# Optimization experiments

Hardware: AMD Instinct MI355X
Metric: run time of the kernel (lower is better)

The kernel has to match this reference:

```python
import jax, jax.numpy as jnp
import numpy as np

B, N, K = 4, 4096, 16
D_POINTS, D_MODEL = 64, 256


def _ln(x, g, b, eps=1e-5):
    mu = jnp.mean(x, axis=-1, keepdims=True)
    var = jnp.mean((x - mu) ** 2, axis=-1, keepdims=True)
    return (x - mu) * jax.lax.rsqrt(var + eps) * g + b


def _gather(points, idx):
    # points: [B,N,C], idx: [B,N,K] -> [B,N,K,C]
    b = jnp.arange(points.shape[0])[:, None, None]
    return points[b, idx]


def setup_inputs() -> dict:
    key = jax.random.key(0)
    ks = jax.random.split(key, 16)
    std_qkv = np.sqrt(2.0 / D_MODEL).astype(np.float32)
    return {
        "xyz": jax.random.normal(ks[0], (B, N, 3), jnp.float32),
        "features": jax.random.normal(ks[1], (B, N, D_POINTS), jnp.float32),
        "W_pre": jax.random.normal(ks[2], (D_MODEL, D_POINTS), jnp.float32) * 0.02,
        "b_pre": jnp.zeros((D_MODEL,), jnp.float32),
        "W_post": jax.random.normal(ks[3], (D_POINTS, D_MODEL), jnp.float32) * 0.02,
        "b_post": jnp.zeros((D_POINTS,), jnp.float32),
        "Wp1": jax.random.normal(ks[4], (D_MODEL, 3), jnp.float32) * 0.02,
        "Wp2": jax.random.normal(ks[5], (D_MODEL, D_MODEL), jnp.float32) * 0.02,
        "Wa1": jax.random.normal(ks[6], (D_MODEL, D_MODEL), jnp.float32) * 0.02,
        "Wa2": jax.random.normal(ks[7], (D_MODEL, D_MODEL), jnp.float32) * 0.02,
        "WQ": jax.random.normal(ks[8], (D_MODEL, D_MODEL), jnp.float32) * std_qkv,
        "WK": jax.random.normal(ks[9], (D_MODEL, D_MODEL), jnp.float32) * std_qkv,
        "WV": jax.random.normal(ks[10], (D_MODEL, D_MODEL), jnp.float32) * std_qkv,
        "Wproj": jax.random.normal(ks[11], (D_MODEL, D_MODEL), jnp.float32) * 0.02,
        "g_dm": jnp.ones((D_MODEL,), jnp.float32),
        "b_dm": jnp.zeros((D_MODEL,), jnp.float32),
        "g_dp": jnp.ones((D_POINTS,), jnp.float32),
        "b_dp": jnp.zeros((D_POINTS,), jnp.float32),
    }


def reference(xyz, features, W_pre, b_pre, W_post, b_post, Wp1, Wp2, Wa1, Wa2,
              WQ, WK, WV, Wproj, g_dm, b_dm, g_dp, b_dp):
    # kNN (state == 'l'): pairwise squared distances, k smallest per point
    dists = jnp.sum((xyz[:, :, None, :] - xyz[:, None, :, :]) ** 2, axis=-1)  # [B,N,N]
    _, idx = jax.lax.top_k(-dists, K)  # [B,N,K] smallest distances (incl. self)

    knn_xyz = _gather(xyz, idx)                      # [B,N,K,3]
    inp = features @ W_pre.T + b_pre                 # [B,N,D]

    q = _ln(inp @ WQ.T, g_dm, b_dm)                  # [B,N,D]
    k_ = _gather(_ln(inp @ WK.T, g_dm, b_dm), idx)   # [B,N,K,D]
    v_ = _gather(_ln(inp @ WV.T, g_dm, b_dm), idx)   # [B,N,K,D]

    rel = xyz[:, :, None, :] - knn_xyz               # [B,N,K,3]
    pos = jax.nn.relu(rel @ Wp1.T) @ Wp2.T           # [B,N,K,D]

    attn = jax.nn.relu((q[:, :, None, :] - k_ + pos) @ Wa1.T) @ Wa2.T  # [B,N,K,D]
    attn = jax.nn.softmax(attn / jnp.sqrt(jnp.float32(D_MODEL)), axis=-2)

    res = jnp.einsum('bnkf,bnkf->bnf', attn, v_ + pos)  # vector attention reduce
    res = _ln(res @ Wproj.T, g_dm, b_dm)
    res = _ln(res @ W_post.T + b_post, g_dp, b_dp) + features
    return res
```

## Files before the change

kernel.cpp:

```cpp
#include <hip/hip_runtime.h>
#include <hip/hip_bf16.h>

typedef unsigned short u16;
typedef unsigned int   u32;
typedef __attribute__((ext_vector_type(8))) short bf16x8;
typedef __attribute__((ext_vector_type(4))) float f32x4;

#define MFMA16(a,b,c) __builtin_amdgcn_mfma_f32_16x16x32_bf16((a),(b),(c),0,0,0)

__device__ __forceinline__ float b2f(u32 h){ return __uint_as_float(h<<16); }
__device__ __forceinline__ u16 f2b(float f){
  u32 u = __float_as_uint(f);
  return (u16)((u + 0x7FFFu + ((u>>16)&1u))>>16);
}
__device__ __forceinline__ u32 pk2f(float a,float b){
  __hip_bfloat162 h = __float22bfloat162_rn(float2{a,b});
  return *reinterpret_cast<u32*>(&h);
}
__device__ __forceinline__ u32 umin32(u32 a,u32 b){ return a<b?a:b; }
__device__ __forceinline__ u32 umax32(u32 a,u32 b){ return a>b?a:b; }

template<int CTRL>
__device__ __forceinline__ float dpp_add(float x){
  int t = __builtin_amdgcn_update_dpp(0, __float_as_int(x), CTRL, 0xF, 0xF, true);
  return x + __int_as_float(t);
}
__device__ __forceinline__ float rowsum16(float x){
  x = dpp_add<0x121>(x);
  x = dpp_add<0x122>(x);
  x = dpp_add<0x124>(x);
  x = dpp_add<0x128>(x);
  return x;
}

__device__ __forceinline__ void async_copy16(const void* g, void* l){
  __builtin_amdgcn_global_load_lds((const __attribute__((address_space(1))) u32*)g,
                                   (__attribute__((address_space(3))) u32*)l, 16, 0, 0);
}

#define OFF_IDX    0ull
#define OFF_WQKV   3178496ull
#define OFF_WA1    3571712ull
#define OFF_WA2    3702784ull
#define OFF_WP2    3833856ull
#define OFF_WPROJ  3964928ull
#define OFF_WPOST  4096000ull
#define OFF_MCOMB  4128768ull
#define OFF_INP    4259840ull
#define OFF_LNQKV  37814272ull
#define OFF_QA     62980096ull
#define OFF_KA     71368704ull
#define OFF_RES    79757312ull
#define OFF_D1     88145920ull
#define WS_NEED    104923136ull
#define OFF_WP1PK  OFF_D1

__device__ __forceinline__ void ins16(u32 (&a)[16], u32 key){
  #pragma unroll
  for (int j = 15; j >= 1; --j) a[j] = umin32(umax32(a[j-1],key), a[j]);
  a[0] = umin32(a[0], key);
}

__device__ __forceinline__ float dist2(float ax,float ay,float az,float bx,float by,float bz){
  const float dx = ax-bx, dy = ay-by, dz = az-bz;
  return __fmaf_rn(dx,dx, __fmaf_rn(dy,dy, dz*dz));
}

__global__ __launch_bounds__(256,2) void prep_k(
    const float* __restrict__ xyz, const float* __restrict__ feat,
    const float* __restrict__ wpre, const float* __restrict__ bpre,
    const float* __restrict__ wq, const float* __restrict__ wk, const float* __restrict__ wv,
    const float* __restrict__ wa1, const float* __restrict__ wa2, const float* __restrict__ wp2,
    const float* __restrict__ wproj, const float* __restrict__ wpost,
    const float* __restrict__ wp1,
    u16* __restrict__ dwqkv, u16* __restrict__ dwa1, u16* __restrict__ dwa2,
    u16* __restrict__ dwp2, u16* __restrict__ dwproj, u16* __restrict__ dwpost,
    u16* __restrict__ dwp1pk, u16* __restrict__ dmcomb,
    int* __restrict__ idxout, u16* __restrict__ dinp){
  __shared__ __attribute__((aligned(16))) char smem[50464];
  const int bid = blockIdx.x, tid = threadIdx.x;
  if (bid < 1856){
    int id = bid*256 + tid;
    const float* s; u16* d; int off;
    if      (id <  65536){ s=wq;    d=dwqkv;        off=id; }
    else if (id < 131072){ s=wk;    d=dwqkv+65536;  off=id-65536; }
    else if (id < 196608){ s=wv;    d=dwqkv+131072; off=id-131072; }
    else if (id < 262144){ s=wa1;   d=dwa1;         off=id-196608; }
    else if (id < 327680){ s=wa2;   d=dwa2;         off=id-262144; }
    else if (id < 393216){ s=wp2;   d=dwp2;         off=id-327680; }
    else if (id < 458752){ s=wproj; d=dwproj;       off=id-393216; }
    else                 { s=wpost; d=dwpost;       off=id-458752; }
    d[off] = f2b(s[off]);
  } else if (bid == 1856){
    const int h = tid;
    const float w0 = wp1[h*3], w1 = wp1[h*3+1], w2 = wp1[h*3+2];
    uint4 a; a.x = pk2f(w0,w1); a.y = pk2f(w2,0.f); a.z = 0u; a.w = 0u;
    uint4 z; z.x = z.y = z.z = z.w = 0u;
    *(uint4*)&dwp1pk[h*32]    = a;
    *(uint4*)&dwp1pk[h*32+8]  = z;
    *(uint4*)&dwp1pk[h*32+16] = z;
    *(uint4*)&dwp1pk[h*32+24] = z;
  } else if (bid < 2113){
    const int f = bid - 1857, h = tid;
    float acc = 0.f;
    #pragma unroll 4
    for (int j = 0; j < 256; ++j) acc = __fmaf_rn(wa1[f*256+j], wp2[j*256+h], acc);
    dmcomb[f*256+h] = f2b(acc);
  } else if (bid < 3137){
    float* sx = (float*)smem; float* sy = sx + 4104; float* sz = sx + 8208;
    int* lcnt   = (int*)(smem + 49248);
    int* tcnt   = (int*)(smem + 49312);
    u32* tbuf   = (u32*)(smem + 49376);
    int* tiebuf = (int*)(smem + 49440);
    const int tb = bid - 2113;
    const int b  = tb >> 8;
    const int n0 = (tb & 255) << 4;
    const float* base = xyz + (size_t)b*12288;
    #pragma unroll
    for (int i = 0; i < 12; ++i){
      const float4 v = *(const float4*)(base + tid*48 + i*4);
      const float vv[4] = {v.x, v.y, v.z, v.w};
      #pragma unroll
      for (int j = 0; j < 4; ++j){
        const int e = i*4 + j;
        const int c = e % 3;
        const int m = tid*16 + e/3;
        float* arr = (c==0)?sx:((c==1)?sy:sz);
        arr[m + (m>>9)] = vv[j];
      }
    }
    if (tid < 16){ lcnt[tid] = 0; tcnt[tid] = 0; }
    __syncthreads();
    const int qi = tid >> 4, p = tid & 15;
    const int n = n0 + qi;
    const int sn = n + (n>>9);
    const float qx = sx[sn], qy = sy[sn], qz = sz[sn];
    u32 a[16];
    #pragma unroll
    for (int j = 0; j < 16; ++j) a[j] = 0xFFFFFFFFu;
    const int sb = p*256 + (p>>1);
    #pragma unroll 2
    for (int i = 0; i < 256; ++i){
      const float d2 = dist2(sx[sb+i],sy[sb+i],sz[sb+i],qx,qy,qz);
      ins16(a, __float_as_uint(d2));
    }
    #pragma unroll
    for (int s = 8; s >= 1; s >>= 1){
      u32 o[16];
      #pragma unroll
      for (int j = 0; j < 16; ++j) o[j] = __shfl_down(a[j], (unsigned)s, 64);
      if (p < s){
        #pragma unroll
        for (int j = 0; j < 16; ++j) ins16(a, o[j]);
      }
    }
    if (p == 0) tbuf[qi] = a[15];
    __syncthreads();
    const u32 T = tbuf[qi];
    int* orow = idxout + ((size_t)(b<<12)+n)*16;
    const int gbase = p*256;
    for (int i = 0; i < 256; ++i){
      const float d2 = dist2(sx[sb+i],sy[sb+i],sz[sb+i],qx,qy,qz);
      const u32 kb = __float_as_uint(d2);
      if (kb < T){
        const int pos = atomicAdd(&lcnt[qi],1);
        if (pos < 16) orow[pos] = gbase + i;
      } else if (kb == T){
        const int t = atomicAdd(&tcnt[qi],1);
        if (t < 16) tiebuf[qi*16+t] = gbase + i;
      }
    }
    __syncthreads();
    if (p == 0){
      int L = lcnt[qi]; if (L > 16) L = 16;
      int tc = tcnt[qi]; if (tc > 16) tc = 16;
      const int need = 16 - L;
      for (int r = 0; r < need; ++r){
        int best = 0x7FFFFFFF, bj = -1;
        for (int j = 0; j < tc; ++j){
          const int v = tiebuf[qi*16+j];
          if (v < best){ best = v; bj = j; }
        }
        if (bj >= 0){ tiebuf[qi*16+bj] = 0x7FFFFFFF; orow[L+r] = best; }
        else orow[L+r] = n;
      }
    }
  } else {
    u16* As = (u16*)smem;
    u16* Bs = (u16*)smem + 9216;
    const int tb = bid - 3137;
    const int mb = tb >> 1, nb = tb & 1;
    #pragma unroll
    for (int i = 0; i < 32; ++i){
      const int e = i*256 + tid;
      const int row = e >> 6, k = e & 63;
      As[row*72+k] = f2b(feat[(size_t)(mb*128)*64 + e]);
      Bs[row*72+k] = f2b(wpre[(size_t)(nb*128)*64 + e]);
    }
    __syncthreads();
    const int lane = tid & 63, w = tid >> 6;
    const int mrow = lane & 15, quad = lane >> 4;
    const int wr = (w&1)*64, wc = (w>>1)*64;
    f32x4 acc[4][4];
    #pragma unroll
    for (int i=0;i<4;++i)
      #pragma unroll
      for (int j=0;j<4;++j)
        #pragma unroll
        for (int r=0;r<4;++r) acc[i][j][r] = 0.f;
    #pragma unroll
    for (int ks = 0; ks < 2; ++ks){
      const int koff = ks*32 + quad*8;
      bf16x8 af[4], bf[4];
      #pragma unroll
      for (int rt=0;rt<4;++rt) af[rt] = *(const bf16x8*)&As[(wr+rt*16+mrow)*72 + koff];
      #pragma unroll
      for (int ct=0;ct<4;++ct) bf[ct] = *(const bf16x8*)&Bs[(wc+ct*16+mrow)*72 + koff];
      #pragma unroll
      for (int rt=0;rt<4;++rt)
        #pragma unroll
        for (int ct=0;ct<4;++ct) acc[rt][ct] = MFMA16(af[rt], bf[ct], acc[rt][ct]);
    }
    #pragma unroll
    for (int rt=0;rt<4;++rt)
      #pragma unroll
      for (int ct=0;ct<4;++ct){
        const size_t row0 = (size_t)mb*128 + wr + rt*16 + quad*4;
        const int col = nb*128 + wc + ct*16 + mrow;
        const float bv = bpre[col];
        #pragma unroll
        for (int r=0;r<4;++r) dinp[(row0+r)*256 + col] = f2b(acc[rt][ct][r] + bv);
      }
  }
}

#define LNP 264
__global__ __launch_bounds__(512,2) void gemmlnqa_k(
    const u16* __restrict__ inp, const u16* __restrict__ wqkv, const u16* __restrict__ wa1,
    u16* __restrict__ qa, u16* __restrict__ ka, u16* __restrict__ lnqkv,
    const float* __restrict__ g, const float* __restrict__ bta){
  __shared__ __attribute__((aligned(16))) u16 As[64*32];
  __shared__ __attribute__((aligned(16))) u16 Bs[256*32];
  __shared__ __attribute__((aligned(16))) u16 lnbuf[64*LNP];
  __shared__ float sS[64], sSS[64];
  const int z = blockIdx.z;
  const u16* wsel = wqkv + z*65536;
  const int tid = threadIdx.x, lane = tid & 63, w = tid >> 6;
  const int mrow = lane & 15, quad = lane >> 4;
  const size_t mbase = (size_t)blockIdx.x*64;
  const int wr = (w&1)*32, wc = (w>>1)*64;
  if (tid < 64){ sS[tid] = 0.f; sSS[tid] = 0.f; }
  f32x4 acc[2][4];
  #pragma unroll
  for (int i=0;i<2;++i)
    #pragma unroll
    for (int j=0;j<4;++j)
      #pragma unroll
      for (int r=0;r<4;++r) acc[i][j][r] = 0.f;
  const int sr = tid >> 2, sk = (tid & 3)*8;
  for (int k0 = 0; k0 < 256; k0 += 32){
    __syncthreads();
    if (tid < 256) async_copy16(inp + (mbase + sr)*256 + k0 + sk, &As[w*512]);
    async_copy16(wsel + (size_t)sr*256       + k0 + sk, &Bs[w*512]);
    async_copy16(wsel + (size_t)(128+sr)*256 + k0 + sk, &Bs[4096 + w*512]);
    __syncthreads();
    bf16x8 af[2], bf[4];
    #pragma unroll
    for (int rt=0;rt<2;++rt) af[rt] = *(const bf16x8*)&As[(wr+rt*16+mrow)*32 + quad*8];
    #pragma unroll
    for (int ct=0;ct<4;++ct) bf[ct] = *(const bf16x8*)&Bs[(wc+ct*16+mrow)*32 + quad*8];
    #pragma unroll
    for (int rt=0;rt<2;++rt)
      #pragma unroll
      for (int ct=0;ct<4;++ct) acc[rt][ct] = MFMA16(af[rt], bf[ct], acc[rt][ct]);
  }
  #pragma unroll
  for (int rt=0;rt<2;++rt)
    #pragma unroll
    for (int r=0;r<4;++r){
      float s  = acc[rt][0][r]+acc[rt][1][r]+acc[rt][2][r]+acc[rt][3][r];
      float ss = acc[rt][0][r]*acc[rt][0][r]+acc[rt][1][r]*acc[rt][1][r]
               + acc[rt][2][r]*acc[rt][2][r]+acc[rt][3][r]*acc[rt][3][r];
      s  = rowsum16(s);
      ss = rowsum16(ss);
      if (mrow == 0){
        const int row = wr + rt*16 + quad*4 + r;
        atomicAdd(&sS[row],  s);
        atomicAdd(&sSS[row], ss);
      }
    }
  __syncthreads();
  #pragma unroll
  for (int ct=0;ct<4;++ct){
    const int col = wc + ct*16 + mrow;
    const float gv = g[col], bv = bta[col];
    #pragma unroll
    for (int rt=0;rt<2;++rt)
      #pragma unroll
      for (int r=0;r<4;++r){
        const int row = wr + rt*16 + quad*4 + r;
        const float mu = sS[row]*(1.f/256.f);
        const float var = sSS[row]*(1.f/256.f) - mu*mu;
        const float rs = rsqrtf(var + 1e-5f);
        const u16 hv = f2b((acc[rt][ct][r]-mu)*rs*gv + bv);
        if (z == 2) lnqkv[(mbase+row)*768 + 512 + col] = hv;
        else        lnbuf[row*LNP + col] = hv;
      }
  }
  if (z == 2) return;
  u16* outp = (z == 0) ? qa : ka;
  f32x4 ac2[2][4];
  #pragma unroll
  for (int i=0;i<2;++i)
    #pragma unroll
    for (int j=0;j<4;++j)
      #pragma unroll
      for (int r=0;r<4;++r) ac2[i][j][r] = 0.f;
  for (int k0 = 0; k0 < 256; k0 += 32){
    __syncthreads();
    async_copy16(wa1 + (size_t)sr*256       + k0 + sk, &Bs[w*512]);
    async_copy16(wa1 + (size_t)(128+sr)*256 + k0 + sk, &Bs[4096 + w*512]);
    __syncthreads();
    bf16x8 af[2], bf[4];
    #pragma unroll
    for (int rt=0;rt<2;++rt) af[rt] = *(const bf16x8*)&lnbuf[(wr+rt*16+mrow)*LNP + k0 + quad*8];
    #pragma unroll
    for (int ct=0;ct<4;++ct) bf[ct] = *(const bf16x8*)&Bs[(wc+ct*16+mrow)*32 + quad*8];
    #pragma unroll
    for (int rt=0;rt<2;++rt)
      #pragma unroll
      for (int ct=0;ct<4;++ct) ac2[rt][ct] = MFMA16(af[rt], bf[ct], ac2[rt][ct]);
  }
  #pragma unroll
  for (int rt=0;rt<2;++rt)
    #pragma unroll
    for (int ct=0;ct<4;++ct){
      const size_t row0 = mbase + wr + rt*16 + quad*4;
      const int col = wc + ct*16 + mrow;
      #pragma unroll
      for (int r=0;r<4;++r) outp[(row0+r)*256 + col] = f2b(ac2[rt][ct][r]);
    }
}

__global__ __launch_bounds__(512,2) void projpost_k(
    const u16* __restrict__ res, const u16* __restrict__ wproj, const u16* __restrict__ wpost,
    const float* __restrict__ bpost,
    const float* __restrict__ g_dm, const float* __restrict__ b_dm,
    const float* __restrict__ g_dp, const float* __restrict__ b_dp,
    const float* __restrict__ feat, float* __restrict__ out){
  __shared__ __attribute__((aligned(16))) u16 As[64*32];
  __shared__ __attribute__((aligned(16))) u16 Bs[256*32];
  __shared__ __attribute__((aligned(16))) u16 lnbuf[64*LNP];
  __shared__ float sS[64], sSS[64], sS2[64], sSS2[64];
  const int tid = threadIdx.x, lane = tid & 63, w = tid >> 6;
  const int mrow = lane & 15, quad = lane >> 4;
  const size_t mbase = (size_t)blockIdx.x*64;
  const int wr = (w&1)*32, wc = (w>>1)*64;
  if (tid < 64){ sS[tid]=0.f; sSS[tid]=0.f; sS2[tid]=0.f; sSS2[tid]=0.f; }
  f32x4 acc[2][4];
  #pragma unroll
  for (int i=0;i<2;++i)
    #pragma unroll
    for (int j=0;j<4;++j)
      #pragma unroll
      for (int r=0;r<4;++r) acc[i][j][r] = 0.f;
  const int sr = tid >> 2, sk = (tid & 3)*8;
  for (int k0 = 0; k0 < 256; k0 += 32){
    __syncthreads();
    if (tid < 256) async_copy16(res + (mbase + sr)*256 + k0 + sk, &As[w*512]);
    async_copy16(wproj + (size_t)sr*256       + k0 + sk, &Bs[w*512]);
    async_copy16(wproj + (size_t)(128+sr)*256 + k0 + sk, &Bs[4096 + w*512]);
    __syncthreads();
    bf16x8 af[2], bf[4];
    #pragma unroll
    for (int rt=0;rt<2;++rt) af[rt] = *(const bf16x8*)&As[(wr+rt*16+mrow)*32 + quad*8];
    #pragma unroll
    for (int ct=0;ct<4;++ct) bf[ct] = *(const bf16x8*)&Bs[(wc+ct*16+mrow)*32 + quad*8];
    #pragma unroll
    for (int rt=0;rt<2;++rt)
      #pragma unroll
      for (int ct=0;ct<4;++ct) acc[rt][ct] = MFMA16(af[rt], bf[ct], acc[rt][ct]);
  }
  #pragma unroll
  for (int rt=0;rt<2;++rt)
    #pragma unroll
    for (int r=0;r<4;++r){
      float s  = acc[rt][0][r]+acc[rt][1][r]+acc[rt][2][r]+acc[rt][3][r];
      float ss = acc[rt][0][r]*acc[rt][0][r]+acc[rt][1][r]*acc[rt][1][r]
               + acc[rt][2][r]*acc[rt][2][r]+acc[rt][3][r]*acc[rt][3][r];
      s  = rowsum16(s);
      ss = rowsum16(ss);
      if (mrow == 0){
        const int row = wr + rt*16 + quad*4 + r;
        atomicAdd(&sS[row],  s);
        atomicAdd(&sSS[row], ss);
      }
    }
  __syncthreads();
  #pragma unroll
  for (int ct=0;ct<4;++ct){
    const int col = wc + ct*16 + mrow;
    const float gv = g_dm[col], bv = b_dm[col];
    #pragma unroll
    for (int rt=0;rt<2;++rt)
      #pragma unroll
      for (int r=0;r<4;++r){
        const int row = wr + rt*16 + quad*4 + r;
        const float mu = sS[row]*(1.f/256.f);
        const float var = sSS[row]*(1.f/256.f) - mu*mu;
        const float rs = rsqrtf(var + 1e-5f);
        lnbuf[row*LNP + col] = f2b((acc[rt][ct][r]-mu)*rs*gv + bv);
      }
  }
  const int wr2 = (w & 3)*16, wc2 = (w >> 2)*32;
  f32x4 ac2[2];
  #pragma unroll
  for (int j=0;j<2;++j)
    #pragma unroll
    for (int r=0;r<4;++r) ac2[j][r] = 0.f;
  for (int k0 = 0; k0 < 256; k0 += 32){
    __syncthreads();
    if (tid < 256) async_copy16(wpost + (size_t)sr*256 + k0 + sk, &Bs[w*512]);
    __syncthreads();
    bf16x8 af, bf[2];
    af = *(const bf16x8*)&lnbuf[(wr2+mrow)*LNP + k0 + quad*8];
    #pragma unroll
    for (int ct=0;ct<2;++ct) bf[ct] = *(const bf16x8*)&Bs[(wc2+ct*16+mrow)*32 + quad*8];
    #pragma unroll
    for (int ct=0;ct<2;++ct) ac2[ct] = MFMA16(af, bf[ct], ac2[ct]);
  }
  #pragma unroll
  for (int ct=0;ct<2;++ct){
    const float bv = bpost[wc2 + ct*16 + mrow];
    #pragma unroll
    for (int r=0;r<4;++r) ac2[ct][r] += bv;
  }
  #pragma unroll
  for (int r=0;r<4;++r){
    float s  = ac2[0][r] + ac2[1][r];
    float ss = ac2[0][r]*ac2[0][r] + ac2[1][r]*ac2[1][r];
    s  = rowsum16(s);
    ss = rowsum16(ss);
    if (mrow == 0){
      const int row = wr2 + quad*4 + r;
      atomicAdd(&sS2[row],  s);
      atomicAdd(&sSS2[row], ss);
    }
  }
  __syncthreads();
  #pragma unroll
  for (int ct=0;ct<2;++ct){
    const int col = wc2 + ct*16 + mrow;
    const float gv = g_dp[col], bv = b_dp[col];
    #pragma unroll
    for (int r=0;r<4;++r){
      const int row = wr2 + quad*4 + r;
      const float mu = sS2[row]*(1.f/64.f);
      const float var = sSS2[row]*(1.f/64.f) - mu*mu;
      const float rs = rsqrtf(var + 1e-5f);
      const size_t grow = mbase + row;
      out[grow*64 + col] = (ac2[ct][r]-mu)*rs*gv + bv + feat[grow*64 + col];
    }
  }
}

#define RELP 40
__device__ __forceinline__ u16* swzp(u16* p, int row, int cb){
  return (u16*)((char*)p + row*512 + (cb ^ ((row & 7) << 4)));
}
__global__ __launch_bounds__(1024,4) void attn_k(
    const float* __restrict__ xyz, const int* __restrict__ idxb,
    const u16* __restrict__ lnqkv, const u16* __restrict__ qa, const u16* __restrict__ ka,
    const u16* __restrict__ mcomb, const u16* __restrict__ wp2, const u16* __restrict__ wa2,
    const u16* __restrict__ wp1pk, u16* __restrict__ res){
  __shared__ __attribute__((aligned(16))) u16 h1buf[128*256];
  __shared__ __attribute__((aligned(16))) u16 h2buf[128*256];
  __shared__ __attribute__((aligned(16))) u16 srel[128*RELP];
  __shared__ int sidx[128];
  const int tid = threadIdx.x;
  const int b = blockIdx.x >> 9;
  const int nbase = (blockIdx.x & 511) << 3;
  const size_t gb = (size_t)b << 12;
  if (tid < 128){
    const int m = tid;
    const int im = idxb[(gb + nbase + (m>>4))*16 + (m&15)] & 4095;
    sidx[m] = im;
    const int nn = nbase + (m>>4);
    const float* pq = xyz + (gb+nn)*3;
    const float* pm = xyz + (gb+im)*3;
    const float rx = pq[0]-pm[0], ry = pq[1]-pm[1], rz = pq[2]-pm[2];
    uint4 a; a.x = pk2f(rx,ry); a.y = pk2f(rz,0.f); a.z = 0u; a.w = 0u;
    uint4 z; z.x = z.y = z.z = z.w = 0u;
    *(uint4*)&srel[m*RELP]    = a;
    *(uint4*)&srel[m*RELP+8]  = z;
    *(uint4*)&srel[m*RELP+16] = z;
    *(uint4*)&srel[m*RELP+24] = z;
  }
  __syncthreads();
  const int lane = tid & 63, w = tid >> 6;
  const int mrow = lane & 15, quad = lane >> 4;
  const int fr = w << 4;
  {
    bf16x8 aW = *(const bf16x8*)&wp1pk[(fr+mrow)*32 + quad*8];
    #pragma unroll
    for (int mt=0;mt<8;++mt){
      bf16x8 bR = *(const bf16x8*)&srel[(mt*16+mrow)*RELP + quad*8];
      f32x4 hz;
      #pragma unroll
      for (int r=0;r<4;++r) hz[r]=0.f;
      hz = MFMA16(aW, bR, hz);
      float h0 = hz[0]>0.f?hz[0]:0.f, h1v = hz[1]>0.f?hz[1]:0.f;
      float h2v = hz[2]>0.f?hz[2]:0.f, h3 = hz[3]>0.f?hz[3]:0.f;
      uint2 o; o.x = pk2f(h0,h1v); o.y = pk2f(h2v,h3);
      *(uint2*)swzp(h1buf, mt*16+mrow, 2*(fr + quad*4)) = o;
    }
  }
  int midx[8];
  #pragma unroll
  for (int mt = 0; mt < 8; ++mt) midx[mt] = sidx[mt*16 + mrow];
  __syncthreads();
  f32x4 at[8], av[8];
  #pragma unroll
  for (int j=0;j<8;++j)
    #pragma unroll
    for (int r=0;r<4;++r){ at[j][r]=0.f; av[j][r]=0.f; }
  #pragma unroll 1
  for (int ks = 0; ks < 8; ++ks){
    const int koff = ks*32 + quad*8;
    bf16x8 aM = *(const bf16x8*)&mcomb[(fr+mrow)*256 + koff];
    bf16x8 aP = *(const bf16x8*)&wp2  [(fr+mrow)*256 + koff];
    #pragma unroll
    for (int mh=0; mh<2; ++mh){
      bf16x8 bH[4];
      #pragma unroll
      for (int mi=0;mi<4;++mi) bH[mi] = *(const bf16x8*)swzp(h1buf, (mh*4+mi)*16+mrow, 2*koff);
      #pragma unroll
      for (int mi=0;mi<4;++mi){
        at[mh*4+mi] = MFMA16(aM, bH[mi], at[mh*4+mi]);
        av[mh*4+mi] = MFMA16(bH[mi], aP, av[mh*4+mi]);
      }
    }
  }
  uint2 qkp[8];
  #pragma unroll
  for (int mt = 0; mt < 8; ++mt){
    const int f = fr + quad*4;
    const uint2 uq = *(const uint2*)&qa[(gb + nbase + mt)*256 + f];
    const uint2 uk = *(const uint2*)&ka[(gb + (size_t)midx[mt])*256 + f];
    uint2 o;
    o.x = pk2f(b2f(uq.x&0xffff)-b2f(uk.x&0xffff), b2f(uq.x>>16)-b2f(uk.x>>16));
    o.y = pk2f(b2f(uq.y&0xffff)-b2f(uk.y&0xffff), b2f(uq.y>>16)-b2f(uk.y>>16));
    qkp[mt] = o;
  }
  #pragma unroll
  for (int mt=0;mt<8;++mt){
    const uint2 qv = qkp[mt];
    float t0 = at[mt][0] + b2f(qv.x&0xffff);
    float t1 = at[mt][1] + b2f(qv.x>>16);
    float t2 = at[mt][2] + b2f(qv.y&0xffff);
    float t3 = at[mt][3] + b2f(qv.y>>16);
    t0 = t0>0.f?t0:0.f; t1 = t1>0.f?t1:0.f; t2 = t2>0.f?t2:0.f; t3 = t3>0.f?t3:0.f;
    uint2 o; o.x = pk2f(t0,t1); o.y = pk2f(t2,t3);
    *(uint2*)swzp(h2buf, mt*16+mrow, 2*(fr + quad*4)) = o;
  }
  __syncthreads();
  {
    #pragma unroll
    for (int i = 0; i < 4; ++i){
      const int row = w*8 + i*2 + (lane>>5);
      const int c   = ((lane&31)*8) ^ ((row & 7) << 3);
      async_copy16(lnqkv + (gb + (size_t)sidx[row])*768 + 512 + c,
                   &h1buf[w*2048 + i*512]);
    }
  }
  f32x4 al[8];
  #pragma unroll
  for (int j=0;j<8;++j)
    #pragma unroll
    for (int r=0;r<4;++r) al[j][r]=0.f;
  #pragma unroll 1
  for (int ks = 0; ks < 8; ++ks){
    const int koff = ks*32 + quad*8;
    bf16x8 aW = *(const bf16x8*)&wa2[(fr+mrow)*256 + koff];
    #pragma unroll
    for (int mh=0; mh<2; ++mh){
      bf16x8 bH[4];
      #pragma unroll
      for (int mi=0;mi<4;++mi) bH[mi] = *(const bf16x8*)swzp(h2buf, (mh*4+mi)*16+mrow, 2*koff);
      #pragma unroll
      for (int mi=0;mi<4;++mi) al[mh*4+mi] = MFMA16(bH[mi], aW, al[mh*4+mi]);
    }
  }
  __syncthreads();
  const float sc = 0.0901684f;
  #pragma unroll
  for (int mt=0;mt<8;++mt){
    float prs = 0.f, wgs = 0.f;
    #pragma unroll
    for (int r=0;r<4;++r){
      const int vr = mt*16 + quad*4 + r;
      const float val = av[mt][r] + b2f((u32)*swzp(h1buf, vr, 2*(fr + mrow)));
      const float pr = exp2f(al[mt][r]*sc);
      prs += pr;
      wgs += pr*val;
    }
    prs += __shfl_xor(prs, 16, 64); prs += __shfl_xor(prs, 32, 64);
    wgs += __shfl_xor(wgs, 16, 64); wgs += __shfl_xor(wgs, 32, 64);
    const float rv = wgs * __builtin_amdgcn_rcpf(prs);
    if (quad == 0)
      res[(gb + nbase + mt)*256 + fr + mrow] = f2b(rv);
  }
}

extern "C" void kernel_launch(void* const* d_in, const int* in_sizes, int n_in,
                              void* d_out, int out_size, void* d_ws, size_t ws_size,
                              hipStream_t stream){
  const float* xyz    = (const float*)d_in[0];
  const float* feat   = (const float*)d_in[1];
  const float* W_pre  = (const float*)d_in[2];
  const float* b_pre  = (const float*)d_in[3];
  const float* W_post = (const float*)d_in[4];
  const float* b_post = (const float*)d_in[5];
  const float* Wp1    = (const float*)d_in[6];
  const float* Wp2    = (const float*)d_in[7];
  const float* Wa1    = (const float*)d_in[8];
  const float* Wa2    = (const float*)d_in[9];
  const float* WQ     = (const float*)d_in[10];
  const float* WK     = (const float*)d_in[11];
  const float* WV     = (const float*)d_in[12];
  const float* Wproj  = (const float*)d_in[13];
  const float* g_dm   = (const float*)d_in[14];
  const float* b_dm   = (const float*)d_in[15];
  const float* g_dp   = (const float*)d_in[16];
  const float* b_dp   = (const float*)d_in[17];
  float* out = (float*)d_out;
  if (ws_size < WS_NEED) return;
  char* ws = (char*)d_ws;
  int* idxw   = (int*)(ws + OFF_IDX);
  u16* wqkvb  = (u16*)(ws + OFF_WQKV);
  u16* wa1b   = (u16*)(ws + OFF_WA1);
  u16* wa2b   = (u16*)(ws + OFF_WA2);
  u16* wp2b   = (u16*)(ws + OFF_WP2);
  u16* wprojb = (u16*)(ws + OFF_WPROJ);
  u16* wpostb = (u16*)(ws + OFF_WPOST);
  u16* mcombb = (u16*)(ws + OFF_MCOMB);
  u16* inp    = (u16*)(ws + OFF_INP);
  u16* lnqkv  = (u16*)(ws + OFF_LNQKV);
  u16* qab    = (u16*)(ws + OFF_QA);
  u16* kab    = (u16*)(ws + OFF_KA);
  u16* resb   = (u16*)(ws + OFF_RES);
  u16* wp1pk  = (u16*)(ws + OFF_WP1PK);

  prep_k<<<3393,256,0,stream>>>(xyz, feat, W_pre, b_pre, WQ, WK, WV, Wa1, Wa2, Wp2,
                                Wproj, W_post, Wp1,
                                wqkvb, wa1b, wa2b, wp2b, wprojb, wpostb,
                                wp1pk, mcombb, idxw, inp);
  gemmlnqa_k<<<dim3(256,1,3),512,0,stream>>>(inp, wqkvb, wa1b, qab, kab, lnqkv, g_dm, b_dm);
  attn_k<<<2048,1024,0,stream>>>(xyz,idxw,lnqkv,qab,kab,mcombb,wp2b,wa2b,wp1pk,resb);
  projpost_k<<<256,512,0,stream>>>(resb, wprojb, wpostb, b_post, g_dm, b_dm, g_dp, b_dp,
                                   feat, out);
}
```

Before: 452.9 us.

## Retile attention kernel waves to 32 features x 4 m-tiles and stage gathered keys in LDS

Each wave now covers 32 output features over half of the 128 neighbor rows, where before it covered 16 features over all rows. Each h1/h2 LDS fragment now feeds two weight tiles, which cuts LDS reads per MFMA, at the cost of twice the global weight-fragment loads per wave. Gathered key rows and query rows are prefetched into LDS with async copies during the first GEMM, replacing the scattered per-lane global uint2 loads that previously followed it. This adds an extra barrier and an 8-row shared query buffer.

```diff
diff --git a/kernel.cpp b/kernel.cpp
--- a/kernel.cpp
+++ b/kernel.cpp
@@ -475,6 +475,7 @@
     const u16* __restrict__ wp1pk, u16* __restrict__ res){
   __shared__ __attribute__((aligned(16))) u16 h1buf[128*256];
   __shared__ __attribute__((aligned(16))) u16 h2buf[128*256];
+  __shared__ __attribute__((aligned(16))) u16 qbuf[8*256];
   __shared__ __attribute__((aligned(16))) u16 srel[128*RELP];
   __shared__ int sidx[128];
   const int tid = threadIdx.x;
@@ -499,70 +500,86 @@
   __syncthreads();
   const int lane = tid & 63, w = tid >> 6;
   const int mrow = lane & 15, quad = lane >> 4;
-  const int fr = w << 4;
+  const int fr   = (w >> 1) << 5;
+  const int mseg = (w & 1) * 4;
   {
-    bf16x8 aW = *(const bf16x8*)&wp1pk[(fr+mrow)*32 + quad*8];
-    #pragma unroll
-    for (int mt=0;mt<8;++mt){
-      bf16x8 bR = *(const bf16x8*)&srel[(mt*16+mrow)*RELP + quad*8];
-      f32x4 hz;
-      #pragma unroll
-      for (int r=0;r<4;++r) hz[r]=0.f;
-      hz = MFMA16(aW, bR, hz);
-      float h0 = hz[0]>0.f?hz[0]:0.f, h1v = hz[1]>0.f?hz[1]:0.f;
-      float h2v = hz[2]>0.f?hz[2]:0.f, h3 = hz[3]>0.f?hz[3]:0.f;
-      uint2 o; o.x = pk2f(h0,h1v); o.y = pk2f(h2v,h3);
-      *(uint2*)swzp(h1buf, mt*16+mrow, 2*(fr + quad*4)) = o;
-    }
-  }
-  int midx[8];
-  #pragma unroll
-  for (int mt = 0; mt < 8; ++mt) midx[mt] = sidx[mt*16 + mrow];
-  __syncthreads();
-  f32x4 at[8], av[8];
-  #pragma unroll
-  for (int j=0;j<8;++j)
-    #pragma unroll
-    for (int r=0;r<4;++r){ at[j][r]=0.f; av[j][r]=0.f; }
+    bf16x8 aW[2];
+    #pragma unroll
+    for (int ft2=0;ft2<2;++ft2) aW[ft2] = *(const bf16x8*)&wp1pk[(fr+ft2*16+mrow)*32 + quad*8];
+    #pragma unroll
+    for (int mi=0;mi<4;++mi){
+      bf16x8 bR = *(const bf16x8*)&srel[((mseg+mi)*16+mrow)*RELP + quad*8];
+      #pragma unroll
+      for (int ft2=0;ft2<2;++ft2){
+        f32x4 hz;
+        #pragma unroll
+        for (int r=0;r<4;++r) hz[r]=0.f;
+        hz = MFMA16(aW[ft2], bR, hz);
+        float h0 = hz[0]>0.f?hz[0]:0.f, h1v = hz[1]>0.f?hz[1]:0.f;
+        float h2v = hz[2]>0.f?hz[2]:0.f, h3 = hz[3]>0.f?hz[3]:0.f;
+        uint2 o; o.x = pk2f(h0,h1v); o.y = pk2f(h2v,h3);
+        *(uint2*)swzp(h1buf, (mseg+mi)*16+mrow, 2*(fr + ft2*16 + quad*4)) = o;
+      }
+    }
+  }
+  __syncthreads();
+  {
+    #pragma unroll
+    for (int i = 0; i < 4; ++i){
+      const int row = w*8 + i*2 + (lane>>5);
+      const int c   = ((lane&31)*8) ^ ((row & 7) << 3);
+      async_copy16(ka + (gb + (size_t)sidx[row])*256 + c,
+                   &h2buf[w*2048 + i*512]);
+    }
+    if (w < 4){
+      const int row = w*2 + (lane>>5);
+      const int c   = ((lane&31)*8) ^ ((row & 7) << 3);
+      async_copy16(qa + (gb + nbase + row)*256 + c, &qbuf[w*512]);
+    }
+  }
+  f32x4 at[2][4], av[2][4];
+  #pragma unroll
+  for (int i=0;i<2;++i)
+    #pragma unroll
+    for (int j=0;j<4;++j)
+      #pragma unroll
+      for (int r=0;r<4;++r){ at[i][j][r]=0.f; av[i][j][r]=0.f; }
   #pragma unroll 1
   for (int ks = 0; ks < 8; ++ks){
     const int koff = ks*32 + quad*8;
-    bf16x8 aM = *(const bf16x8*)&mcomb[(fr+mrow)*256 + koff];
-    bf16x8 aP = *(const bf16x8*)&wp2  [(fr+mrow)*256 + koff];
-    #pragma unroll
-    for (int mh=0; mh<2; ++mh){
-      bf16x8 bH[4];
-      #pragma unroll
-      for (int mi=0;mi<4;++mi) bH[mi] = *(const bf16x8*)swzp(h1buf, (mh*4+mi)*16+mrow, 2*koff);
+    bf16x8 aM[2], aP[2], bH[4];
+    #pragma unroll
+    for (int ft2=0;ft2<2;++ft2){
+      aM[ft2] = *(const bf16x8*)&mcomb[(fr+ft2*16+mrow)*256 + koff];
+      aP[ft2] = *(const bf16x8*)&wp2  [(fr+ft2*16+mrow)*256 + koff];
+    }
+    #pragma unroll
+    for (int mi=0;mi<4;++mi) bH[mi] = *(const bf16x8*)swzp(h1buf, (mseg+mi)*16+mrow, 2*koff);
+    #pragma unroll
+    for (int ft2=0;ft2<2;++ft2)
       #pragma unroll
       for (int mi=0;mi<4;++mi){
-        at[mh*4+mi] = MFMA16(aM, bH[mi], at[mh*4+mi]);
-        av[mh*4+mi] = MFMA16(bH[mi], aP, av[mh*4+mi]);
-      }
-    }
-  }
-  uint2 qkp[8];
-  #pragma unroll
-  for (int mt = 0; mt < 8; ++mt){
-    const int f = fr + quad*4;
-    const uint2 uq = *(const uint2*)&qa[(gb + nbase + mt)*256 + f];
-    const uint2 uk = *(const uint2*)&ka[(gb + (size_t)midx[mt])*256 + f];
-    uint2 o;
-    o.x = pk2f(b2f(uq.x&0xffff)-b2f(uk.x&0xffff), b2f(uq.x>>16)-b2f(uk.x>>16));
-    o.y = pk2f(b2f(uq.y&0xffff)-b2f(uk.y&0xffff), b2f(uq.y>>16)-b2f(uk.y>>16));
-    qkp[mt] = o;
-  }
-  #pragma unroll
-  for (int mt=0;mt<8;++mt){
-    const uint2 qv = qkp[mt];
-    float t0 = at[mt][0] + b2f(qv.x&0xffff);
-    float t1 = at[mt][1] + b2f(qv.x>>16);
-    float t2 = at[mt][2] + b2f(qv.y&0xffff);
-    float t3 = at[mt][3] + b2f(qv.y>>16);
-    t0 = t0>0.f?t0:0.f; t1 = t1>0.f?t1:0.f; t2 = t2>0.f?t2:0.f; t3 = t3>0.f?t3:0.f;
-    uint2 o; o.x = pk2f(t0,t1); o.y = pk2f(t2,t3);
-    *(uint2*)swzp(h2buf, mt*16+mrow, 2*(fr + quad*4)) = o;
-  }
+        at[ft2][mi] = MFMA16(aM[ft2], bH[mi], at[ft2][mi]);
+        av[ft2][mi] = MFMA16(bH[mi], aP[ft2], av[ft2][mi]);
+      }
+  }
+  __syncthreads();
+  #pragma unroll
+  for (int ft2=0;ft2<2;++ft2)
+    #pragma unroll
+    for (int mi=0;mi<4;++mi){
+      const int cb = 2*(fr + ft2*16 + quad*4);
+      u16* addr = swzp(h2buf, (mseg+mi)*16+mrow, cb);
+      const uint2 kv = *(const uint2*)addr;
+      const uint2 qv = *(const uint2*)swzp(qbuf, mseg+mi, cb);
+      float t0 = at[ft2][mi][0] + b2f(qv.x&0xffff) - b2f(kv.x&0xffff);
+      float t1 = at[ft2][mi][1] + b2f(qv.x>>16)    - b2f(kv.x>>16);
+      float t2 = at[ft2][mi][2] + b2f(qv.y&0xffff) - b2f(kv.y&0xffff);
+      float t3 = at[ft2][mi][3] + b2f(qv.y>>16)    - b2f(kv.y>>16);
+      t0 = t0>0.f?t0:0.f; t1 = t1>0.f?t1:0.f; t2 = t2>0.f?t2:0.f; t3 = t3>0.f?t3:0.f;
+      uint2 o; o.x = pk2f(t0,t1); o.y = pk2f(t2,t3);
+      *(uint2*)addr = o;
+    }
   __syncthreads();
   {
     #pragma unroll
@@ -573,43 +590,47 @@
                    &h1buf[w*2048 + i*512]);
     }
   }
-  f32x4 al[8];
-  #pragma unroll
-  for (int j=0;j<8;++j)
-    #pragma unroll
-    for (int r=0;r<4;++r) al[j][r]=0.f;
+  f32x4 al[2][4];
+  #pragma unroll
+  for (int i=0;i<2;++i)
+    #pragma unroll
+    for (int j=0;j<4;++j)
+      #pragma unroll
+      for (int r=0;r<4;++r) al[i][j][r]=0.f;
   #pragma unroll 1
   for (int ks = 0; ks < 8; ++ks){
     const int koff = ks*32 + quad*8;
-    bf16x8 aW = *(const bf16x8*)&wa2[(fr+mrow)*256 + koff];
-    #pragma unroll
-    for (int mh=0; mh<2; ++mh){
-      bf16x8 bH[4];
-      #pragma unroll
-      for (int mi=0;mi<4;++mi) bH[mi] = *(const bf16x8*)swzp(h2buf, (mh*4+mi)*16+mrow, 2*koff);
-      #pragma unroll
-      for (int mi=0;mi<4;++mi) al[mh*4+mi] = MFMA16(bH[mi], aW, al[mh*4+mi]);
-    }
+    bf16x8 aW[2], bH[4];
+    #pragma unroll
+    for (int ft2=0;ft2<2;++ft2) aW[ft2] = *(const bf16x8*)&wa2[(fr+ft2*16+mrow)*256 + koff];
+    #pragma unroll
+    for (int mi=0;mi<4;++mi) bH[mi] = *(const bf16x8*)swzp(h2buf, (mseg+mi)*16+mrow, 2*koff);
+    #pragma unroll
+    for (int ft2=0;ft2<2;++ft2)
+      #pragma unroll
+      for (int mi=0;mi<4;++mi) al[ft2][mi] = MFMA16(bH[mi], aW[ft2], al[ft2][mi]);
   }
   __syncthreads();
   const float sc = 0.0901684f;
   #pragma unroll
-  for (int mt=0;mt<8;++mt){
-    float prs = 0.f, wgs = 0.f;
-    #pragma unroll
-    for (int r=0;r<4;++r){
-      const int vr = mt*16 + quad*4 + r;
-      const float val = av[mt][r] + b2f((u32)*swzp(h1buf, vr, 2*(fr + mrow)));
-      const float pr = exp2f(al[mt][r]*sc);
-      prs += pr;
-      wgs += pr*val;
-    }
-    prs += __shfl_xor(prs, 16, 64); prs += __shfl_xor(prs, 32, 64);
-    wgs += __shfl_xor(wgs, 16, 64); wgs += __shfl_xor(wgs, 32, 64);
-    const float rv = wgs * __builtin_amdgcn_rcpf(prs);
-    if (quad == 0)
-      res[(gb + nbase + mt)*256 + fr + mrow] = f2b(rv);
-  }
+  for (int ft2=0;ft2<2;++ft2)
+    #pragma unroll
+    for (int mi=0;mi<4;++mi){
+      float prs = 0.f, wgs = 0.f;
+      #pragma unroll
+      for (int r=0;r<4;++r){
+        const int vr = (mseg+mi)*16 + quad*4 + r;
+        const float val = av[ft2][mi][r] + b2f((u32)*swzp(h1buf, vr, 2*(fr + ft2*16 + mrow)));
+        const float pr = exp2f(al[ft2][mi][r]*sc);
+        prs += pr;
+        wgs += pr*val;
+      }
+      prs += __shfl_xor(prs, 16, 64); prs += __shfl_xor(prs, 32, 64);
+      wgs += __shfl_xor(wgs, 16, 64); wgs += __shfl_xor(wgs, 32, 64);
+      const float rv = wgs * __builtin_amdgcn_rcpf(prs);
+      if (quad == 0)
+        res[(gb + nbase + mseg + mi)*256 + fr + ft2*16 + mrow] = f2b(rv);
+    }
 }
 
 extern "C" void kernel_launch(void* const* d_in, const int* in_sizes, int n_in,
```

New measurement: 527.4 us. 1.16x slower.
